# Performance work log

Measured on AMD Instinct MI355X. Metric: run time of the kernel, lower is better.

The kernel has to match this reference:

```python
import jax, jax.numpy as jnp
import numpy as np

ETA = 0.01   # nudging rate from __init__ default
EPS = 1e-8   # cosine-similarity epsilon


def setup_inputs() -> dict:
    key = jax.random.key(0)
    ks = jax.random.split(key, 6)
    B, F, S, E, D = 64, 512, 8192, 500000, 1024
    return {
        "heatmap_features_batch": jax.random.normal(ks[0], (B, F), dtype=jnp.float32),
        "grad_output_batch": jax.random.normal(ks[1], (B, F), dtype=jnp.float32),
        "sign_features": jax.random.normal(ks[2], (S, F), dtype=jnp.float32),
        "edge_weight": jax.random.uniform(ks[3], (E,), dtype=jnp.float32),
        "edge_disease": jax.random.randint(ks[4], (E,), 0, D, dtype=jnp.int32),
        "edge_sign": jax.random.randint(ks[5], (E,), 0, S, dtype=jnp.int32),
        "num_diseases": D,
    }


def reference(heatmap_features_batch, grad_output_batch, sign_features,
              edge_weight, edge_disease, edge_sign, num_diseases):
    # Cosine similarity between every sample's heatmap feature vector and every
    # sign node's stored feature vector, rescaled to [0, 1].
    Hn = heatmap_features_batch / (
        jnp.linalg.norm(heatmap_features_batch, axis=1, keepdims=True) + EPS)
    Sn = sign_features / (
        jnp.linalg.norm(sign_features, axis=1, keepdims=True) + EPS)
    sim = (jnp.einsum('bf,sf->bs', Hn, Sn) + 1.0) * 0.5          # [B, S]

    # Per-edge weighted similarity, gathered at each edge's sign node.
    contrib = sim[:, edge_sign] * edge_weight[None, :]           # [B, E]

    # Scatter-add edge contributions into the disease (source) index.
    agg = jax.ops.segment_sum(contrib.T, edge_disease,
                              num_segments=num_diseases)         # [D, B]

    # Per-sample gradient norm factor g^(i) = ||grad_i||_2.
    gnorm = jnp.linalg.norm(grad_output_batch, axis=1)           # [B]

    return ETA * gnorm[:, None] * agg.T                          # [B, D]
```

## Files before the change

kernel.cpp:

```cpp
#include <hip/hip_runtime.h>
#include <math.h>

#define EPS 1e-8f
#define SCB 256
#define NG1 128
#define CAP 768

typedef __attribute__((ext_vector_type(8))) __bf16 bf16x8;
typedef __attribute__((ext_vector_type(4))) float f32x4;

__device__ __forceinline__ unsigned short f2bf(float x) {
    unsigned int u = __float_as_uint(x);
    u += 0x7FFFu + ((u >> 16) & 1u);
    return (unsigned short)(u >> 16);
}
__device__ __forceinline__ unsigned int pack2(float lo, float hi) {
    return (unsigned int)f2bf(lo) | ((unsigned int)f2bf(hi) << 16);
}

__global__ __launch_bounds__(256) void k_norms(
        const float* __restrict__ Sg, const float* __restrict__ Hg,
        const float* __restrict__ Gg, unsigned short* __restrict__ Sgb,
        unsigned short* __restrict__ Hsb, float* __restrict__ gscale,
        int* __restrict__ cursor, int Srows, int Fdim, int Bdim, int Dd) {
    __shared__ float redA[4][17];
    __shared__ float redB[4][17];
    int bid = blockIdx.x;
    int tid = threadIdx.x;
    int lane = tid & 63, wv = tid >> 6;
    int r = tid & 15, cg = tid >> 4;
    int nsT = Srows >> 4;

    if (bid < nsT + (Bdim >> 4)) {
        bool isH = bid >= nsT;
        int t = isH ? bid - nsT : bid;
        const float* basep = isH ? Hg : Sg;
        const float4* src = (const float4*)(basep + ((size_t)t * 16 + r) * Fdim);

        float4 v[8];
        float ss = 0.f, sgq = 0.f;
        #pragma unroll
        for (int g = 0; g < 4; g++) {
            int c = cg + g * 16;
            float4 x = src[c * 2], y = src[c * 2 + 1];
            v[2 * g] = x; v[2 * g + 1] = y;
            ss += x.x * x.x + x.y * x.y + x.z * x.z + x.w * x.w
                + y.x * y.x + y.y * y.y + y.z * y.z + y.w * y.w;
        }
        if (isH) {
            const float4* srcg = (const float4*)(Gg + ((size_t)t * 16 + r) * Fdim);
            #pragma unroll
            for (int g = 0; g < 4; g++) {
                int c = cg + g * 16;
                float4 x = srcg[c * 2], y = srcg[c * 2 + 1];
                sgq += x.x * x.x + x.y * x.y + x.z * x.z + x.w * x.w
                     + y.x * y.x + y.y * y.y + y.z * y.z + y.w * y.w;
            }
        }
        ss  += __shfl_xor(ss, 16, 64);  ss  += __shfl_xor(ss, 32, 64);
        sgq += __shfl_xor(sgq, 16, 64); sgq += __shfl_xor(sgq, 32, 64);
        if (lane < 16) { redA[wv][lane] = ss; redB[wv][lane] = sgq; }
        __syncthreads();
        float tot = redA[0][r] + redA[1][r] + redA[2][r] + redA[3][r];
        float rv = 1.0f / (sqrtf(tot) + EPS);
        if (isH && tid < 16) {
            float tg = redB[0][tid] + redB[1][tid] + redB[2][tid] + redB[3][tid];
            gscale[t * 16 + tid] = 0.005f * sqrtf(tg);
        }
        uint4* dp = (uint4*)(isH ? Hsb : Sgb);
        #pragma unroll
        for (int g = 0; g < 4; g++) {
            int c = cg + g * 16;
            uint4 o;
            o.x = pack2(v[2 * g].x * rv,     v[2 * g].y * rv);
            o.y = pack2(v[2 * g].z * rv,     v[2 * g].w * rv);
            o.z = pack2(v[2 * g + 1].x * rv, v[2 * g + 1].y * rv);
            o.w = pack2(v[2 * g + 1].z * rv, v[2 * g + 1].w * rv);
            dp[(size_t)t * 1024 + (size_t)c * 16 + r] = o;
        }
    } else {
        for (int i = tid; i < Dd; i += 256) cursor[i] = 0;
    }
}

__global__ __launch_bounds__(256) void k_g1scat(
        const unsigned short* __restrict__ Sgb,
        const unsigned short* __restrict__ Hsb, float* __restrict__ Pt,
        const int* __restrict__ ed, const int* __restrict__ es,
        const float* __restrict__ ew, int* __restrict__ cursor,
        int2* __restrict__ sorted, int Srows, int Fdim, int E, int Dd) {
    __shared__ int cnt[1024];
    int id = blockIdx.x;
    int tid = threadIdx.x;

    if (id < NG1) {
        int lane = tid & 63, w = tid >> 6;
        int wt = id * 4 + w;
        const bf16x8* A  = (const bf16x8*)Sgb + (size_t)wt * 1024 + lane;
        const bf16x8* Bp = (const bf16x8*)Hsb + lane;

        bf16x8 a[16];
        #pragma unroll
        for (int kt = 0; kt < 16; kt++) a[kt] = A[kt * 64];

        f32x4 acc0 = {0.f, 0.f, 0.f, 0.f};
        f32x4 acc1 = {0.f, 0.f, 0.f, 0.f};
        f32x4 acc2 = {0.f, 0.f, 0.f, 0.f};
        f32x4 acc3 = {0.f, 0.f, 0.f, 0.f};

        bf16x8 b0 = Bp[0], b1 = Bp[1024], b2 = Bp[2048], b3 = Bp[3072];
        #pragma unroll
        for (int kt = 0; kt < 16; kt++) {
            bf16x8 c0 = b0, c1 = b1, c2 = b2, c3 = b3;
            if (kt < 15) {
                int o = (kt + 1) * 64;
                b0 = Bp[o];        b1 = Bp[o + 1024];
                b2 = Bp[o + 2048]; b3 = Bp[o + 3072];
            }
            acc0 = __builtin_amdgcn_mfma_f32_16x16x32_bf16(a[kt], c0, acc0, 0, 0, 0);
            acc1 = __builtin_amdgcn_mfma_f32_16x16x32_bf16(a[kt], c1, acc1, 0, 0, 0);
            acc2 = __builtin_amdgcn_mfma_f32_16x16x32_bf16(a[kt], c2, acc2, 0, 0, 0);
            acc3 = __builtin_amdgcn_mfma_f32_16x16x32_bf16(a[kt], c3, acc3, 0, 0, 0);
        }
        int r16 = lane & 15, q = lane >> 4;
        int s0 = wt * 16;
        #pragma unroll
        for (int rr = 0; rr < 4; rr++) {
            int s = s0 + q * 4 + rr;
            float* row = Pt + (size_t)s * 64 + r16;
            row[0]  = acc0[rr];
            row[16] = acc1[rr];
            row[32] = acc2[rr];
            row[48] = acc3[rr];
        }
    } else {
        int h = id - NG1;
        for (int i = tid; i < Dd; i += 256) cnt[i] = 0;
        __syncthreads();
        int chunk = (E + SCB - 1) / SCB;
        int e0 = h * chunk;
        int e1 = min(E, e0 + chunk);
        int myd[8], mys[8], myr[8];
        float myw[8];
        #pragma unroll
        for (int i = 0; i < 8; i++) {
            int e = e0 + tid + i * 256;
            myd[i] = -1;
            if (e < e1) {
                myd[i] = ed[e]; mys[i] = es[e]; myw[i] = ew[e];
                myr[i] = atomicAdd(&cnt[myd[i]], 1);
            }
        }
        __syncthreads();
        for (int d = tid; d < Dd; d += 256) {
            int c = cnt[d];
            if (c) cnt[d] = atomicAdd(&cursor[d], c);
        }
        __syncthreads();
        #pragma unroll
        for (int i = 0; i < 8; i++) {
            if (myd[i] >= 0) {
                int pos = cnt[myd[i]] + myr[i];
                sorted[(size_t)myd[i] * CAP + pos] =
                    make_int2(mys[i], __float_as_int(myw[i]));
            }
        }
    }
}

__global__ __launch_bounds__(256) void k_gather(
        const int2* __restrict__ sorted, const float* __restrict__ Pt,
        const int* __restrict__ cursor, const float* __restrict__ gscale,
        float* __restrict__ out, int Dd) {
    __shared__ float sacc[4][64];
    __shared__ float scs[4];
    int d = blockIdx.x;
    int tid = threadIdx.x;
    int lane = tid & 63, w = tid >> 6;
    int cnt = cursor[d];
    const int2* sp = sorted + (size_t)d * CAP;
    float acc = 0.f, cs = 0.f;
    #pragma unroll 8
    for (int i = w; i < cnt; i += 4) {
        int2 p = sp[i];
        float wt = __int_as_float(p.y);
        acc += wt * Pt[(size_t)p.x * 64 + lane];
        cs += wt;
    }
    sacc[w][lane] = acc;
    if (lane == 0) scs[w] = cs;
    __syncthreads();
    if (tid < 64) {
        float a = sacc[0][tid] + sacc[1][tid] + sacc[2][tid] + sacc[3][tid]
                + scs[0] + scs[1] + scs[2] + scs[3];
        out[(size_t)tid * Dd + d] = gscale[tid] * a;
    }
}

extern "C" void kernel_launch(void* const* d_in, const int* in_sizes, int n_in,
                              void* d_out, int out_size, void* d_ws, size_t ws_size,
                              hipStream_t stream) {
    const float* H  = (const float*)d_in[0];
    const float* G  = (const float*)d_in[1];
    const float* Sg = (const float*)d_in[2];
    const float* ew = (const float*)d_in[3];
    const int*   ed = (const int*)d_in[4];
    const int*   es = (const int*)d_in[5];

    const int B = 64;
    const int F = in_sizes[0] / B;
    const int S = in_sizes[2] / F;
    const int E = in_sizes[3];
    const int D = out_size / B;
    float* out = (float*)d_out;

    float* ws = (float*)d_ws;
    size_t off = 0;
    unsigned short* Sgb = (unsigned short*)(ws + off); off += (size_t)S * F / 2;
    unsigned short* Hsb = (unsigned short*)(ws + off); off += (size_t)B * F / 2;
    float* gscale = ws + off; off += 256;
    float* Pt     = ws + off; off += (size_t)S * B;
    int*   cursor = (int*)(ws + off); off += (size_t)D;
    int2*  sorted = (int2*)(ws + off); off += 2 * (size_t)D * CAP;

    k_norms<<<S / 16 + B / 16 + 1, 256, 0, stream>>>(Sg, H, G, Sgb, Hsb, gscale,
                                                     cursor, S, F, B, D);
    k_g1scat<<<NG1 + SCB, 256, 0, stream>>>(Sgb, Hsb, Pt, ed, es, ew,
                                            cursor, sorted, S, F, E, D);
    k_gather<<<D, 256, 0, stream>>>(sorted, Pt, cursor, gscale, out, D);
}
```

Before: 119.8 us.

## Use fewer, larger scatter blocks and double-buffer B-operand prefetch in GEMM

The edge bucketing now runs on 64 blocks instead of 256. Each block loops over its larger chunk twice: first counting edges into shared memory, then re-reading the edges and using shared atomics to assign slots. This cuts the global cursor atomics and trades register-held edge data for a second pass over the edge arrays. Separately, the MFMA loop prefetches B operands two k-steps ahead with two register sets, to hide more load latency at the cost of extra registers.

```diff
diff --git a/kernel.cpp b/kernel.cpp
--- a/kernel.cpp
+++ b/kernel.cpp
@@ -2,7 +2,7 @@
 #include <math.h>
 
 #define EPS 1e-8f
-#define SCB 256
+#define SCB 64
 #define NG1 128
 #define CAP 768
 
@@ -108,14 +108,22 @@
         f32x4 acc2 = {0.f, 0.f, 0.f, 0.f};
         f32x4 acc3 = {0.f, 0.f, 0.f, 0.f};
 
-        bf16x8 b0 = Bp[0], b1 = Bp[1024], b2 = Bp[2048], b3 = Bp[3072];
+        bf16x8 b0a = Bp[0],  b1a = Bp[1024], b2a = Bp[2048], b3a = Bp[3072];
+        bf16x8 b0b = Bp[64], b1b = Bp[1088], b2b = Bp[2112], b3b = Bp[3136];
         #pragma unroll
         for (int kt = 0; kt < 16; kt++) {
-            bf16x8 c0 = b0, c1 = b1, c2 = b2, c3 = b3;
-            if (kt < 15) {
-                int o = (kt + 1) * 64;
-                b0 = Bp[o];        b1 = Bp[o + 1024];
-                b2 = Bp[o + 2048]; b3 = Bp[o + 3072];
+            bf16x8 c0, c1, c2, c3;
+            if ((kt & 1) == 0) { c0 = b0a; c1 = b1a; c2 = b2a; c3 = b3a; }
+            else               { c0 = b0b; c1 = b1b; c2 = b2b; c3 = b3b; }
+            if (kt < 14) {
+                int o = (kt + 2) * 64;
+                if ((kt & 1) == 0) {
+                    b0a = Bp[o];        b1a = Bp[o + 1024];
+                    b2a = Bp[o + 2048]; b3a = Bp[o + 3072];
+                } else {
+                    b0b = Bp[o];        b1b = Bp[o + 1024];
+                    b2b = Bp[o + 2048]; b3b = Bp[o + 3072];
+                }
             }
             acc0 = __builtin_amdgcn_mfma_f32_16x16x32_bf16(a[kt], c0, acc0, 0, 0, 0);
             acc1 = __builtin_amdgcn_mfma_f32_16x16x32_bf16(a[kt], c1, acc1, 0, 0, 0);
@@ -140,30 +148,18 @@
         int chunk = (E + SCB - 1) / SCB;
         int e0 = h * chunk;
         int e1 = min(E, e0 + chunk);
-        int myd[8], mys[8], myr[8];
-        float myw[8];
-        #pragma unroll
-        for (int i = 0; i < 8; i++) {
-            int e = e0 + tid + i * 256;
-            myd[i] = -1;
-            if (e < e1) {
-                myd[i] = ed[e]; mys[i] = es[e]; myw[i] = ew[e];
-                myr[i] = atomicAdd(&cnt[myd[i]], 1);
-            }
-        }
+        for (int e = e0 + tid; e < e1; e += 256)
+            atomicAdd(&cnt[ed[e]], 1);
         __syncthreads();
         for (int d = tid; d < Dd; d += 256) {
             int c = cnt[d];
-            if (c) cnt[d] = atomicAdd(&cursor[d], c);
-        }
-        __syncthreads();
-        #pragma unroll
-        for (int i = 0; i < 8; i++) {
-            if (myd[i] >= 0) {
-                int pos = cnt[myd[i]] + myr[i];
-                sorted[(size_t)myd[i] * CAP + pos] =
-                    make_int2(mys[i], __float_as_int(myw[i]));
-            }
+            cnt[d] = c ? atomicAdd(&cursor[d], c) : 0;
+        }
+        __syncthreads();
+        for (int e = e0 + tid; e < e1; e += 256) {
+            int d = ed[e];
+            int pos = atomicAdd(&cnt[d], 1);
+            sorted[(size_t)d * CAP + pos] = make_int2(es[e], __float_as_int(ew[e]));
         }
     }
 }
```

New measurement: 132.6 us. 10.7% more time.
